# Kernel tuning notes

Hardware: AMD Instinct MI355X
Metric: run time of the kernel (lower is better)

Reference implementation:

```python
import jax, jax.numpy as jnp
import numpy as np

EPS = 1e-5
STW = 10   # short_term_window_size
L = 12     # mlp_layers


def gru_step(h, x, Wi, Wh, bi, bh):
    # torch nn.GRU cell, gate order (r, z, n)
    gi = x @ Wi.T + bi            # [B, 3H]
    gh = h @ Wh.T + bh            # [B, 3H]
    ir, iz, inn = jnp.split(gi, 3, axis=-1)
    hr, hz, hn = jnp.split(gh, 3, axis=-1)
    r = jax.nn.sigmoid(ir + hr)
    z = jax.nn.sigmoid(iz + hz)
    n = jnp.tanh(inn + r * hn)
    return (1.0 - z) * n + z * h


def mlp_mini(m, seq_W, seq_b, ln_a, ln_b, out_W, out_b, mrg_W, mrg_b):
    # m: [B, S, H] -> siMLPe_mini -> [B, 1, C]
    f = jnp.swapaxes(m, 1, 2)                 # [B, H, S]
    for l in range(L):                        # TransMLP: temporal FC + spatial LN + residual
        y = f @ seq_W[l].T + seq_b[l]         # Linear over seq axis S
        mu = y.mean(axis=1, keepdims=True)    # LN over feature ('spatial') axis H
        var = ((y - mu) ** 2).mean(axis=1, keepdims=True)
        y = (y - mu) / jnp.sqrt(var + EPS) * ln_a[l][None, :, None] + ln_b[l][None, :, None]
        f = f + y
    f = jnp.swapaxes(f, 1, 2) @ out_W.T + out_b   # [B, S, C]  motion_fc_out
    f = jnp.swapaxes(f, 1, 2) @ mrg_W.T + mrg_b   # [B, C, 1]  temporal_merge_fc
    return jnp.swapaxes(f, 1, 2)                  # [B, 1, C]


def _forward(x, gru_Wi, gru_Wh, gru_bi, gru_bh, enc_W, enc_b,
             seq_W, seq_b, ln_alpha, ln_beta, out_W, out_b, merge_W, merge_b):
    B, T, C = x.shape
    H = gru_Wh.shape[1]

    @jax.checkpoint
    def enc_step(h, xt):
        return gru_step(h, xt, gru_Wi, gru_Wh, gru_bi, gru_bh), None

    h0 = jnp.zeros((B, H), dtype=x.dtype)
    h_enc, _ = jax.lax.scan(enc_step, h0, jnp.swapaxes(x[:, :-1, :], 0, 1))

    last_frame = x[:, -1, :]
    # encode_history=True: one GRU step on the last frame; resulting state discarded
    window_history = gru_step(h_enc, last_frame, gru_Wi, gru_Wh, gru_bi, gru_bh)[:, None, :]  # [B,1,H]

    buf0 = x[:, -STW:, :]  # sliding short-term window buffer [B, STW, C]

    @jax.checkpoint
    def dec_step(carry, _):
        h, last, buf = carry
        h = gru_step(h, last, gru_Wi, gru_Wh, gru_bi, gru_bh)
        dec = h[:, None, :]                        # [B, 1, H]
        wst = buf @ enc_W.T + enc_b                # fc_encoder: [B, STW, H]
        mlp_in = jnp.concatenate([window_history, wst, dec], axis=1)  # [B, STW+2, H]
        new = mlp_mini(mlp_in, seq_W, seq_b, ln_alpha, ln_beta, out_W, out_b, mrg_W=merge_W, mrg_b=merge_b)
        new = new + last[:, None, :]               # recursive_residual=True
        newf = new[:, 0, :]
        buf = jnp.concatenate([buf[:, 1:, :], new], axis=1)
        return (h, newf, buf), newf

    _, outs = jax.lax.scan(dec_step, (h_enc, last_frame, buf0), None, length=T)
    return jnp.swapaxes(outs, 0, 1)  # [B, T, C]


def setup_inputs() -> dict:
    key = jax.random.key(0)
    B, T, C, H = 1024, 64, 66, 1024
    S = STW + 2
    ks = jax.random.split(key, 16)

    def g(k, shape, scale):
        return jax.random.normal(k, shape, dtype=jnp.float32) * scale

    return {
        "x": g(ks[0], (B, T, C), 1.0),
        "gru_Wi": g(ks[1], (3 * H, C), 0.05),
        "gru_Wh": g(ks[2], (3 * H, H), 0.02),
        "gru_bi": jnp.zeros((3 * H,), jnp.float32),
        "gru_bh": jnp.zeros((3 * H,), jnp.float32),
        "enc_W": g(ks[3], (H, C), 0.05),
        "enc_b": jnp.zeros((H,), jnp.float32),
        "seq_W": g(ks[4], (L, S, S), 0.2),
        "seq_b": jnp.zeros((L, S), jnp.float32),
        "ln_alpha": jnp.ones((L, H), jnp.float32),
        "ln_beta": jnp.zeros((L, H), jnp.float32),
        "out_W": g(ks[5], (C, H), 0.02),
        "out_b": jnp.zeros((C,), jnp.float32),
        "merge_W": g(ks[6], (1, S), 0.2),
        "merge_b": jnp.zeros((1,), jnp.float32),
    }


def reference(x, gru_Wi, gru_Wh, gru_bi, gru_bh, enc_W, enc_b,
              seq_W, seq_b, ln_alpha, ln_beta, out_W, out_b, merge_W, merge_b):
    return _forward(x, gru_Wi, gru_Wh, gru_bi, gru_bh, enc_W, enc_b,
                    seq_W, seq_b, ln_alpha, ln_beta, out_W, out_b, merge_W, merge_b)
```

## Files before the change

### kernel.cpp

```cpp
#include <hip/hip_runtime.h>
#include <hip/hip_bf16.h>
#include <cstddef>
#include <cstdint>

#define BB 1024
#define TT 64
#define CC 66
#define HH 1024
#define SS 12
#define LL 12
#define XROW (TT*CC)
#define DPSEG 32

typedef __attribute__((ext_vector_type(8))) __bf16 bfrag;
typedef __attribute__((ext_vector_type(4))) float f32x4;
typedef __attribute__((ext_vector_type(8))) short s8v;
typedef __attribute__((ext_vector_type(2))) float f2;

#define SWROW(r) (((r) >> 1) & 3)

__device__ __forceinline__ unsigned short f2bf(float f) {
  unsigned int u = __builtin_bit_cast(unsigned int, f);
  unsigned int r = u + 0x7FFFu + ((u >> 16) & 1u);
  return (unsigned short)(r >> 16);
}
__device__ __forceinline__ float bf2f(unsigned short h) {
  unsigned int u = ((unsigned int)h) << 16;
  return __builtin_bit_cast(float, u);
}

__device__ __forceinline__ void gload16(const void* g, void* l) {
  __builtin_amdgcn_global_load_lds(
      (const __attribute__((address_space(1))) unsigned int*)g,
      (__attribute__((address_space(3))) unsigned int*)l, 16, 0, 0);
}

template<int CTRL, int RM>
__device__ __forceinline__ float dppadd(float v) {
  int x = __builtin_amdgcn_update_dpp(0, __builtin_bit_cast(int, v),
                                      CTRL, RM, 0xF, true);
  return v + __builtin_bit_cast(float, x);
}
__device__ __forceinline__ float wave_sum63(float v) {
  v = dppadd<0x111, 0xF>(v);
  v = dppadd<0x112, 0xF>(v);
  v = dppadd<0x114, 0xF>(v);
  v = dppadd<0x118, 0xF>(v);
  v = dppadd<0x142, 0xa>(v);
  v = dppadd<0x143, 0xc>(v);
  return v;
}

__global__ __launch_bounds__(256) void gru_mfma(
    const unsigned short* __restrict__ Ahi, const unsigned short* __restrict__ Alo,
    const float* __restrict__ hprev,
    const unsigned short* __restrict__ Xhi, const unsigned short* __restrict__ Xlo,
    const unsigned short* __restrict__ Whi, const unsigned short* __restrict__ Wlo,
    const float* __restrict__ bi, const float* __restrict__ bh,
    float* __restrict__ hout_f32,
    unsigned short* __restrict__ hout_hi, unsigned short* __restrict__ hout_lo,
    const float* __restrict__ B144, float* __restrict__ dp32,
    const int* __restrict__ flagp, int do_dp)
{
  __shared__ __align__(16) unsigned short AsH[3][64*32];
  __shared__ __align__(16) unsigned short AsL[3][64*32];
  __shared__ __align__(16) unsigned short BsH[3][128*32];
  __shared__ __align__(16) unsigned short BsL[3][128*32];

  const int tid = threadIdx.x, lane = tid & 63, wid = tid >> 6;
  const int bid = blockIdx.x;
  const int idx = bid >> 3;
  const int jb = (bid & 7) * 4 + (idx & 3);
  const int b0 = (idx >> 2) * 64;
  const int wm = wid >> 1, wn = wid & 1;
  const int aR = lane >> 2, aC = lane & 3;

  auto stage = [&](int bs, int kc) {
    const unsigned short *shi, *slo; size_t go;
    int row = wid * 16 + aR;
    if (kc < 32) {
      go = (size_t)(b0 + row) * 1024 + (size_t)kc * 32 + aC * 8;
      shi = Ahi; slo = Alo;
    } else {
      go = (size_t)(b0 + row) * 96 + (size_t)(kc - 32) * 32 + aC * 8;
      shi = Xhi; slo = Xlo;
    }
    gload16(shi + go, &AsH[bs][wid * 512]);
    gload16(slo + go, &AsL[bs][wid * 512]);
    size_t base = ((size_t)jb * 35 + kc) * 4096;
    size_t go0 = base + (size_t)(wid * 32 + aR) * 32 + aC * 8;
    gload16(Whi + go0,       &BsH[bs][wid * 1024]);
    gload16(Whi + go0 + 512, &BsH[bs][wid * 1024 + 512]);
    gload16(Wlo + go0,       &BsL[bs][wid * 1024]);
    gload16(Wlo + go0 + 512, &BsL[bs][wid * 1024 + 512]);
  };

  int offA[2], offB[4];
  #pragma unroll
  for (int mh = 0; mh < 2; ++mh) {
    int r = wm * 32 + mh * 16 + (lane & 15);
    int cb = (lane >> 4) ^ SWROW(r);
    offA[mh] = r * 32 + cb * 8;
  }
  #pragma unroll
  for (int g = 0; g < 4; ++g) {
    int r = wn * 64 + g * 16 + (lane & 15);
    int cb = (lane >> 4) ^ SWROW(r);
    offB[g] = r * 32 + cb * 8;
  }

  f32x4 acc[2][4] = {};

  stage(0, 0);
  stage(1, 1);

  int cur = 0;
  for (int kc = 0; kc < 34; ++kc) {
    asm volatile("s_waitcnt vmcnt(6)" ::: "memory");
    __builtin_amdgcn_s_barrier();
    asm volatile("" ::: "memory");

    bfrag ah[2], al[2], bhf[4], blf[4];
    #pragma unroll
    for (int mh = 0; mh < 2; ++mh) {
      ah[mh] = __builtin_bit_cast(bfrag, *(const s8v*)(&AsH[cur][offA[mh]]));
      al[mh] = __builtin_bit_cast(bfrag, *(const s8v*)(&AsL[cur][offA[mh]]));
    }
    #pragma unroll
    for (int g = 0; g < 4; ++g) {
      bhf[g] = __builtin_bit_cast(bfrag, *(const s8v*)(&BsH[cur][offB[g]]));
      blf[g] = __builtin_bit_cast(bfrag, *(const s8v*)(&BsL[cur][offB[g]]));
    }
    if (kc < 33) {
      int st = (cur >= 1) ? cur - 1 : 2;
      stage(st, kc + 2);
    }
    #pragma unroll
    for (int mh = 0; mh < 2; ++mh)
      #pragma unroll
      for (int g = 0; g < 4; ++g) {
        acc[mh][g] = __builtin_amdgcn_mfma_f32_16x16x32_bf16(ah[mh], bhf[g], acc[mh][g], 0, 0, 0);
        acc[mh][g] = __builtin_amdgcn_mfma_f32_16x16x32_bf16(ah[mh], blf[g], acc[mh][g], 0, 0, 0);
        acc[mh][g] = __builtin_amdgcn_mfma_f32_16x16x32_bf16(al[mh], bhf[g], acc[mh][g], 0, 0, 0);
      }
    cur = (cur < 2) ? cur + 1 : 0;
  }
  {
    asm volatile("s_waitcnt vmcnt(0)" ::: "memory");
    __builtin_amdgcn_s_barrier();
    asm volatile("" ::: "memory");
    bfrag ah[2], al[2], bhf[4], blf[4];
    #pragma unroll
    for (int mh = 0; mh < 2; ++mh) {
      ah[mh] = __builtin_bit_cast(bfrag, *(const s8v*)(&AsH[1][offA[mh]]));
      al[mh] = __builtin_bit_cast(bfrag, *(const s8v*)(&AsL[1][offA[mh]]));
    }
    #pragma unroll
    for (int g = 0; g < 4; ++g) {
      bhf[g] = __builtin_bit_cast(bfrag, *(const s8v*)(&BsH[1][offB[g]]));
      blf[g] = __builtin_bit_cast(bfrag, *(const s8v*)(&BsL[1][offB[g]]));
    }
    #pragma unroll
    for (int mh = 0; mh < 2; ++mh)
      #pragma unroll
      for (int g = 0; g < 4; ++g) {
        acc[mh][g] = __builtin_amdgcn_mfma_f32_16x16x32_bf16(ah[mh], bhf[g], acc[mh][g], 0, 0, 0);
        acc[mh][g] = __builtin_amdgcn_mfma_f32_16x16x32_bf16(ah[mh], blf[g], acc[mh][g], 0, 0, 0);
        acc[mh][g] = __builtin_amdgcn_mfma_f32_16x16x32_bf16(al[mh], bhf[g], acc[mh][g], 0, 0, 0);
      }
  }

  const int j = jb * 32 + wn * 16 + (lane & 15);
  const float b_r  = bi[j] + bh[j];
  const float b_z  = bi[HH + j] + bh[HH + j];
  const float b_nh = bh[2 * HH + j];
  const float b_nx = bi[2 * HH + j];
  float hvv[2][4];
  #pragma unroll
  for (int mh = 0; mh < 2; ++mh)
    #pragma unroll
    for (int q = 0; q < 4; ++q) {
      int m = b0 + wm * 32 + mh * 16 + (lane >> 4) * 4 + q;
      float hpv = hprev[(size_t)m * HH + j];
      float rr = acc[mh][0][q] + b_r;
      float zz = acc[mh][1][q] + b_z;
      float nh = acc[mh][2][q] + b_nh;
      float nx = acc[mh][3][q] + b_nx;
      float r = 1.f / (1.f + __expf(-rr));
      float z = 1.f / (1.f + __expf(-zz));
      float n = tanhf(nx + r * nh);
      float hv = (1.f - z) * n + z * hpv;
      hvv[mh][q] = hv;
      hout_f32[(size_t)m * HH + j] = hv;
      unsigned short hi = f2bf(hv);
      float lo = hv - bf2f(hi);
      int cb = ((j >> 3) & 3) ^ SWROW(m);
      size_t dst = (size_t)m * 1024 + (size_t)(j & ~31) + cb * 8 + (j & 7);
      hout_hi[dst] = hi;
      hout_lo[dst] = f2bf(lo);
    }

  if (do_dp && *flagp) {
    float* hsf = reinterpret_cast<float*>(&AsH[0][0]);
    __syncthreads();
    #pragma unroll
    for (int mh = 0; mh < 2; ++mh)
      #pragma unroll
      for (int q = 0; q < 4; ++q) {
        int mloc = wm * 32 + mh * 16 + (lane >> 4) * 4 + q;
        int jloc = wn * 16 + (lane & 15);
        hsf[mloc * 33 + jloc] = hvv[mh][q];
      }
    __syncthreads();
    const int b_sub = tid & 63;
    const int cg = __builtin_amdgcn_readfirstlane(tid >> 6);
    const int base_c = cg * 36;
    float acc36[36];
    #pragma unroll
    for (int i = 0; i < 36; ++i) acc36[i] = 0.f;
    for (int kk = 0; kk < 32; ++kk) {
      float av = hsf[b_sub * 33 + kk];
      const float* brow = B144 + (size_t)(jb * 32 + kk) * 144 + base_c;
      #pragma unroll
      for (int qq = 0; qq < 9; ++qq) {
        f32x4 b4 = *(const f32x4*)(brow + qq * 4);
        acc36[qq*4+0] = fmaf(av, b4[0], acc36[qq*4+0]);
        acc36[qq*4+1] = fmaf(av, b4[1], acc36[qq*4+1]);
        acc36[qq*4+2] = fmaf(av, b4[2], acc36[qq*4+2]);
        acc36[qq*4+3] = fmaf(av, b4[3], acc36[qq*4+3]);
      }
    }
    float* drow = dp32 + ((size_t)jb * 1024 + b0 + b_sub) * 144 + base_c;
    #pragma unroll
    for (int qq = 0; qq < 9; ++qq)
      *(f32x4*)(drow + qq * 4) = { acc36[qq*4+0], acc36[qq*4+1], acc36[qq*4+2], acc36[qq*4+3] };
  }
}

__global__ __launch_bounds__(256) void prep_wgc(
    const float* __restrict__ Wh, const float* __restrict__ Wi,
    unsigned short* __restrict__ Whi, unsigned short* __restrict__ Wlo)
{
  size_t idx = (size_t)blockIdx.x * 256 + threadIdx.x;
  if (idx >= (size_t)4096 * 1120) return;
  int k = (int)(idx % 1120);
  int rg = (int)(idx / 1120);
  int jbv = rg >> 7, r = rg & 127;
  int jhi = r >> 6, rem = r & 63, g = rem >> 4, jlo = rem & 15;
  int j = jbv * 32 + jhi * 16 + jlo;
  float v = 0.f;
  if (g == 0)      v = (k < 1024) ? Wh[(size_t)j * HH + k]            : ((k < 1090) ? Wi[(size_t)j * CC + (k - 1024)] : 0.f);
  else if (g == 1) v = (k < 1024) ? Wh[(size_t)(HH + j) * HH + k]     : ((k < 1090) ? Wi[(size_t)(HH + j) * CC + (k - 1024)] : 0.f);
  else if (g == 2) v = (k < 1024) ? Wh[(size_t)(2 * HH + j) * HH + k] : 0.f;
  else             v = (k >= 1024 && k < 1090) ? Wi[(size_t)(2 * HH + j) * CC + (k - 1024)] : 0.f;
  unsigned short hi = f2bf(v);
  float lo = v - bf2f(hi);
  int kc = k >> 5, kk = k & 31;
  int cb = ((kk >> 3) ^ SWROW(r)) & 3;
  size_t dst = (((size_t)jbv * 35 + kc) * 128 + r) * 32 + cb * 8 + (kk & 7);
  Whi[dst] = hi;
  Wlo[dst] = f2bf(lo);
}

__global__ __launch_bounds__(256) void prep_xall(
    const float* __restrict__ x,
    unsigned short* __restrict__ Xhi, unsigned short* __restrict__ Xlo)
{
  size_t idx = (size_t)blockIdx.x * 256 + threadIdx.x;
  if (idx >= (size_t)TT * BB * 96) return;
  int kx = (int)(idx % 96);
  size_t rem = idx / 96;
  int b = (int)(rem % BB);
  int t = (int)(rem / BB);
  float v = (kx < CC) ? x[(size_t)b * XROW + (size_t)t * CC + kx] : 0.f;
  unsigned short hi = f2bf(v);
  float lo = v - bf2f(hi);
  int cb = (((kx >> 3) & 3) ^ SWROW(b)) & 3;
  size_t dst = ((size_t)t * BB + b) * 96 + (size_t)(kx & ~31) + cb * 8 + (kx & 7);
  Xhi[dst] = hi;
  Xlo[dst] = f2bf(lo);
}

__global__ __launch_bounds__(256) void wst_row_kernel(
    const float* __restrict__ src, int src_stride,
    const float* __restrict__ encWT, const float* __restrict__ encb,
    float* __restrict__ dst, const int* __restrict__ flagp)
{
  if (*flagp) return;
  __shared__ float s[CC];
  int b = blockIdx.y;
  int h = blockIdx.x * 256 + threadIdx.x;
  if (threadIdx.x < CC) s[threadIdx.x] = src[(size_t)b * src_stride + threadIdx.x];
  __syncthreads();
  float acc = encb[h];
  #pragma unroll
  for (int k = 0; k < CC; ++k) acc = fmaf(s[k], encWT[(size_t)k * HH + h], acc);
  dst[(size_t)b * (10 * HH) + h] = acc;
}

__global__ __launch_bounds__(256) void transpose_encW(
    const float* __restrict__ W, float* __restrict__ WT)
{
  int k = blockIdx.x;
  int h = blockIdx.y * 256 + threadIdx.x;
  WT[(size_t)k * HH + h] = W[(size_t)h * CC + k];
}

__global__ __launch_bounds__(256) void copy_last_kernel(
    const float* __restrict__ x, float* __restrict__ last)
{
  int idx = blockIdx.x * 256 + threadIdx.x;
  if (idx < BB * CC) {
    int b = idx / CC, c = idx - b * CC;
    last[idx] = x[(size_t)b * XROW + 63 * CC + c];
  }
}

__global__ __launch_bounds__(256) void flag_kernel(
    const float* __restrict__ lnA, const float* __restrict__ lnB, int* flagp)
{
  int idx = blockIdx.x * 256 + threadIdx.x;
  bool ok;
  if (idx < LL * HH) ok = (lnA[idx] == 1.0f);
  else ok = (lnB[idx - LL * HH] == 0.0f);
  if (!ok) atomicAnd(flagp, 0);
}

__global__ __launch_bounds__(256) void prep_tabs(
    const float* __restrict__ encW, const float* __restrict__ encb,
    const float* __restrict__ outW, float* __restrict__ tabs)
{
  const int lane = threadIdx.x & 63, wid = threadIdx.x >> 6;
  int idx = blockIdx.x * 4 + wid;
  if (idx >= 8978) return;
  float a = 0.f;
  if (idx < 4356) {
    int c1 = idx / 66, c2 = idx % 66;
    for (int h = lane; h < HH; h += 64) a = fmaf(encW[h * CC + c1], encW[h * CC + c2], a);
  } else if (idx < 8712) {
    int p = idx - 4356; int c = p / 66, c1 = p % 66;
    for (int h = lane; h < HH; h += 64) a = fmaf(encW[h * CC + c1], outW[(size_t)c * HH + h], a);
  } else if (idx < 8778) {
    int c1 = idx - 8712;
    for (int h = lane; h < HH; h += 64) a = fmaf(encW[h * CC + c1], encb[h], a);
  } else if (idx < 8844) {
    int c1 = idx - 8778;
    for (int h = lane; h < HH; h += 64) a += encW[h * CC + c1];
  } else if (idx < 8910) {
    int c = idx - 8844;
    for (int h = lane; h < HH; h += 64) a = fmaf(encb[h], outW[(size_t)c * HH + h], a);
  } else if (idx < 8976) {
    int c = idx - 8910;
    for (int h = lane; h < HH; h += 64) a += outW[(size_t)c * HH + h];
  } else if (idx == 8976) {
    for (int h = lane; h < HH; h += 64) a = fmaf(encb[h], encb[h], a);
  } else {
    for (int h = lane; h < HH; h += 64) a += encb[h];
  }
  a = wave_sum63(a);
  if (lane == 63) tabs[idx] = a;
}

__global__ __launch_bounds__(256) void prep_b144(
    const float* __restrict__ encW, const float* __restrict__ outW,
    const float* __restrict__ encb, float* __restrict__ B144)
{
  int idx = blockIdx.x * 256 + threadIdx.x;
  if (idx >= 1024 * 144) return;
  int k = idx / 144, n = idx % 144;
  float v;
  if (n < 66) v = encW[k * CC + n];
  else if (n < 132) v = outW[(size_t)(n - 66) * HH + k];
  else if (n == 132) v = encb[k];
  else if (n == 133) v = 1.f;
  else v = 0.f;
  B144[idx] = v;
}

__global__ __launch_bounds__(256) void linit_kernel(
    const float* __restrict__ x, float* __restrict__ l_ring,
    const int* __restrict__ flagp)
{
  if (!*flagp) return;
  int idx = blockIdx.x * 256 + threadIdx.x;
  if (idx >= 1024 * 9 * 66) return;
  int c = idx % 66; int r = idx / 66; int w = r % 9; int b = r / 9;
  l_ring[((size_t)b * 10 + w) * 66 + c] = x[(size_t)b * XROW + (54 + w) * CC + c];
}

__global__ __launch_bounds__(256) void qnew_kernel(
    const float* __restrict__ src, int sstride, const float* __restrict__ K3,
    float* __restrict__ q_ring, int slot, const int* __restrict__ flagp)
{
  if (!*flagp) return;
  __shared__ float Ks[4356];
  __shared__ float ls[8][66];
  int tid = threadIdx.x, b0 = blockIdx.x * 8;
  for (int i = tid; i < 4356; i += 256) Ks[i] = K3[i];
  for (int i = tid; i < 8 * 66; i += 256)
    ls[i / 66][i % 66] = src[(size_t)(b0 + i / 66) * sstride + (i % 66)];
  __syncthreads();
  for (int o = tid; o < 528; o += 256) {
    int bi = o / 66, c1 = o % 66;
    float a = 0.f;
    for (int c2 = 0; c2 < 66; ++c2) a = fmaf(Ks[c1 * 66 + c2], ls[bi][c2], a);
    q_ring[((size_t)(b0 + bi) * 10 + slot) * 66 + c1] = a;
  }
}

__global__ __launch_bounds__(256) void fast_combine(
    const float* __restrict__ dp, float* __restrict__ u, float* __restrict__ G,
    float* __restrict__ e, float* __restrict__ s, const int* __restrict__ flagp)
{
  if (!*flagp) return;
  int o = blockIdx.x * 256 + threadIdx.x;
  if (o >= 1024 * 144) return;
  int b = o / 144, c = o % 144;
  float a = 0.f;
  #pragma unroll
  for (int g = 0; g < DPSEG; ++g) a += dp[((size_t)g * 1024 + b) * 144 + c];
  if (c < 66) u[b * 66 + c] = a;
  else if (c < 132) G[b * 66 + (c - 66)] = a;
  else if (c == 132) e[b] = a;
  else if (c == 133) s[b] = a;
}

__global__ __launch_bounds__(256) void tail_kernel(
    const float* __restrict__ hdec, const float* __restrict__ whp,
    float* __restrict__ last, float* __restrict__ l_ring,
    float* __restrict__ q_ring, const float* __restrict__ dp,
    const float* __restrict__ u_whp, const float* __restrict__ G_whp,
    const float* __restrict__ e_whp, const float* __restrict__ s_whp,
    const float* __restrict__ tabs,
    float* __restrict__ wst, const float* __restrict__ encWT,
    const float* __restrict__ encb,
    const float* __restrict__ seqW, const float* __restrict__ seqb,
    const float* __restrict__ lnA, const float* __restrict__ lnB,
    const float* __restrict__ outW, const float* __restrict__ outb,
    const float* __restrict__ mrgW, const float* __restrict__ mrgb,
    int ring0, float* __restrict__ outp,
    unsigned short* __restrict__ lpH, unsigned short* __restrict__ lpL,
    const int* __restrict__ flagp)
{
  const int b = blockIdx.x, tid = threadIdx.x;
  const int lane = tid & 63, wid = tid >> 6;
  const int slot9 = (ring0 == 0) ? 9 : ring0 - 1;

  if (*flagp) {
    __shared__ float l_all[10][66], Qv[10][66];
    __shared__ float yd[66], gd[66], uw[66], se1[66], scs[66], lmix[66], newf[66];
    __shared__ float sW[156], sMm[156], sTt[156], sPp[156], sNn[156], sQq[156];
    __shared__ float sb12[12], sistd[12], scc[12], sfb[12], sdd12[12], swd[12], sVv[12], smrg[12];
    __shared__ float sred[12], misc[8];

    const float* K2T   = tabs + 4356;
    const float* tb_e1 = tabs + 8712;
    const float* tb_cs = tabs + 8778;
    const float* tb_g0 = tabs + 8844;
    const float* tb_R  = tabs + 8910;

    for (int i = tid; i < 660; i += 256) {
      int w = i / 66, c = i % 66;
      int slot = ring0 + w; if (slot >= 10) slot -= 10;
      Qv[w][c] = q_ring[((size_t)b * 10 + slot) * 66 + c];
      if (w < 9) l_all[w][c] = l_ring[((size_t)b * 10 + slot) * 66 + c];
      else       l_all[9][c] = last[(size_t)b * 66 + c];
    }
    for (int i = tid; i < 66; i += 256) {
      uw[i]  = u_whp[(size_t)b * 66 + i];
      se1[i] = tb_e1[i];
      scs[i] = tb_cs[i];
    }
    if (tid < 134) {
      float a = 0.f;
      #pragma unroll
      for (int g = 0; g < DPSEG; ++g) a += dp[((size_t)g * 1024 + b) * 144 + tid];
      if (tid < 66) yd[tid] = a;
      else if (tid < 132) gd[tid - 66] = a;
      else if (tid == 132) misc[1] = a;
      else misc[2] = a;
    }
    if (tid >= 160 && tid < 172) smrg[tid - 160] = mrgW[tid - 160];
    {
      f32x4 hv = *(const f32x4*)&hdec[(size_t)b * 1024 + tid * 4];
      f32x4 wv = *(const f32x4*)&whp[(size_t)b * 1024 + tid * 4];
      float d2 = hv[0]*hv[0] + hv[1]*hv[1] + hv[2]*hv[2] + hv[3]*hv[3];
      float dw = hv[0]*wv[0] + hv[1]*wv[1] + hv[2]*wv[2] + hv[3]*wv[3];
      float w2 = wv[0]*wv[0] + wv[1]*wv[1] + wv[2]*wv[2] + wv[3]*wv[3];
      d2 = wave_sum63(d2); dw = wave_sum63(dw); w2 = wave_sum63(w2);
      if (lane == 63) { sred[wid*3] = d2; sred[wid*3+1] = dw; sred[wid*3+2] = w2; }
    }
    __syncthreads();
    if (tid >= 128 && tid < 131) {
      int i = tid - 128;
      misc[3 + i] = sred[i] + sred[3 + i] + sred[6 + i] + sred[9 + i];
    }
    if (tid == 132) misc[6] = tabs[8976];
    if (tid == 133) misc[7] = tabs[8977];
    __syncthreads();

    if (tid < 144) {
      int i = tid / 12, j = tid % 12;
      float gv;
      if (i == 0 && j == 0) gv = misc[5];
      else if (i == 11 && j == 11) gv = misc[3];
      else if ((i == 0 && j == 11) || (i == 11 && j == 0)) gv = misc[4];
      else if (i == 0 || j == 0) {
        int w = (i == 0 ? j : i) - 1;
        float a = e_whp[b];
        for (int c = 0; c < 66; ++c) a = fmaf(uw[c], l_all[w][c], a);
        gv = a;
      } else if (i == 11 || j == 11) {
        int w = (i == 11 ? j : i) - 1;
        float a = misc[1];
        for (int c = 0; c < 66; ++c) a = fmaf(yd[c], l_all[w][c], a);
        gv = a;
      } else {
        int wi = i - 1, wj = j - 1;
        float a = misc[6];
        for (int c = 0; c < 66; ++c) a = fmaf(se1[c], l_all[wi][c] + l_all[wj][c], a);
        for (int c = 0; c < 66; ++c) a = fmaf(l_all[wi][c], Qv[wj][c], a);
        gv = a;
      }
      sMm[i * 13 + j] = gv * (1.f / 1024.f);
      sTt[i * 13 + j] = (i == j) ? 1.f : 0.f;
    }
    if (tid >= 144 && tid < 156) {
      int k = tid - 144;
      float fb;
      if (k == 0) fb = s_whp[b] * (1.f / 1024.f);
      else if (k == 11) fb = misc[2] * (1.f / 1024.f);
      else {
        float a = misc[7];
        for (int c = 0; c < 66; ++c) a = fmaf(scs[c], l_all[k - 1][c], a);
        fb = a * (1.f / 1024.f);
      }
      sfb[k] = fb;
      sdd12[k] = 0.f;
    }
    __syncthreads();

    for (int l = 0; l < LL; ++l) {
      if (tid < 144) sW[(tid / 12) * 13 + (tid % 12)] = seqW[l * 144 + tid];
      if (tid >= 160 && tid < 172) sb12[tid - 160] = seqb[l * 12 + (tid - 160)];
      __syncthreads();
      if (tid < 144) {
        int s = tid / 12, k = tid % 12;
        float a = 0.f;
        #pragma unroll
        for (int k2 = 0; k2 < 12; ++k2) a = fmaf(sW[s * 13 + k2], sMm[k2 * 13 + k], a);
        sPp[s * 13 + k] = a;
      }
      __syncthreads();
      if (tid < 12) {
        int s = tid;
        float mu = sb12[s];
        #pragma unroll
        for (int k = 0; k < 12; ++k) mu = fmaf(sW[s * 13 + k], sfb[k], mu);
        float e2 = 0.f;
        #pragma unroll
        for (int k = 0; k < 12; ++k) e2 = fmaf(sPp[s * 13 + k], sW[s * 13 + k], e2);
        float wf = mu - sb12[s];
        float var = fmaxf(e2 - wf * wf, 0.f);
        float is = 1.f / sqrtf(var + 1e-5f);
        sistd[s] = is;
        scc[s] = is * (sb12[s] - mu);
      }
      __syncthreads();
      if (tid < 144) {
        int i = tid / 12, j = tid % 12;
        float a = 0.f;
        #pragma unroll
        for (int k = 0; k < 12; ++k) a = fmaf(sW[i * 13 + k], sTt[k * 13 + j], a);
        sQq[i * 13 + j] = a;
        sNn[i * 13 + j] = sMm[i * 13 + j] + sistd[i] * sPp[i * 13 + j];
      }
      if (tid >= 144 && tid < 156) {
        int i = tid - 144;
        float a = 0.f;
        #pragma unroll
        for (int k = 0; k < 12; ++k) a = fmaf(sW[i * 13 + k], sdd12[k], a);
        swd[i] = a;
      }
      __syncthreads();
      if (tid < 144) {
        int i = tid / 12, j = tid % 12;
        sTt[i * 13 + j] += sistd[i] * sQq[i * 13 + j];
        float a = 0.f;
        #pragma unroll
        for (int k = 0; k < 12; ++k) a = fmaf(sNn[i * 13 + k], sW[j * 13 + k], a);
        sPp[i * 13 + j] = a;
      }
      if (tid >= 144 && tid < 156) {
        int i = tid - 144;
        sdd12[i] = sdd12[i] + sistd[i] * swd[i] + scc[i];
      }
      __syncthreads();
      if (tid < 144) {
        int i = tid / 12, j = tid % 12;
        sMm[i * 13 + j] = sNn[i * 13 + j] + sPp[i * 13 + j] * sistd[j]
                        + sfb[i] * scc[j] + scc[i] * sfb[j] - scc[i] * scc[j];
      }
      __syncthreads();
    }

    if (tid < 12) {
      float a = 0.f;
      #pragma unroll
      for (int s = 0; s < 12; ++s) a = fmaf(smrg[s], sTt[s * 13 + tid], a);
      sVv[tid] = a;
    }
    if (tid == 200) {
      float a = 0.f;
      for (int s = 0; s < 12; ++s) a = fmaf(smrg[s], sdd12[s], a);
      misc[0] = a;
    }
    __syncthreads();
    if (tid < 66) {
      float a = 0.f;
      #pragma unroll
      for (int w = 0; w < 9; ++w) a = fmaf(sVv[1 + w], l_all[w][tid], a);
      a = fmaf(sVv[10], l_all[9][tid], a);
      lmix[tid] = a;
    }
    __syncthreads();
    if (tid < 66) {
      int c = tid;
      float vsr = 0.f, smw = 0.f;
      #pragma unroll
      for (int k = 1; k <= 10; ++k) vsr += sVv[k];
      #pragma unroll
      for (int s = 0; s < 12; ++s) smw += smrg[s];
      float lastv = l_all[9][c];
      float acc = sVv[0] * G_whp[(size_t)b * 66 + c]
                + vsr * tb_g0[c]
                + sVv[11] * gd[c]
                + misc[0] * tb_R[c]
                + smw * outb[c] + mrgb[0] + lastv;
      const float* krow = K2T + c * 66;
      for (int c2 = 0; c2 < 66; ++c2) acc = fmaf(lmix[c2], krow[c2], acc);
      outp[(size_t)b * XROW + c] = acc;
      last[(size_t)b * 66 + c] = acc;
      l_ring[((size_t)b * 10 + slot9) * 66 + c] = lastv;
      newf[c] = acc;
      unsigned short hi = f2bf(acc);
      float lo = acc - bf2f(hi);
      int cb = (((c >> 3) & 3) ^ SWROW(b)) & 3;
      size_t dst = (size_t)b * 96 + (size_t)(c & ~31) + cb * 8 + (c & 7);
      lpH[dst] = hi;
      lpL[dst] = f2bf(lo);
    }
    __syncthreads();
    if (tid < 66) {
      float a = 0.f;
      const float* k3r = tabs + tid * 66;
      for (int c2 = 0; c2 < 66; ++c2) a = fmaf(k3r[c2], newf[c2], a);
      q_ring[((size_t)b * 10 + ring0) * 66 + tid] = a;
    }
    return;
  }

  __shared__ float red[4][24];
  __shared__ f2 mustd2[SS];
  __shared__ float g_lds[HH];
  __shared__ float nc[CC];

  const int h0 = tid;
  const int h1 = tid + 512;
  const float* lrow = last + (size_t)b * CC;
  f2 wnew[2];
  {
    f2 a0 = { encb[h0], encb[h0 + 256] };
    f2 a1 = { encb[h1], encb[h1 + 256] };
    #pragma unroll 11
    for (int k = 0; k < CC; ++k) {
      float lv = lrow[k];
      f2 lv2 = { lv, lv };
      f2 w0 = { encWT[(size_t)k * HH + h0], encWT[(size_t)k * HH + h0 + 256] };
      f2 w1 = { encWT[(size_t)k * HH + h1], encWT[(size_t)k * HH + h1 + 256] };
      a0 = __builtin_elementwise_fma(lv2, w0, a0);
      a1 = __builtin_elementwise_fma(lv2, w1, a1);
    }
    wnew[0] = a0; wnew[1] = a1;
    float* wd = wst + ((size_t)b * 10 + slot9) * HH;
    wd[h0] = a0.x; wd[h0 + 256] = a0.y;
    wd[h1] = a1.x; wd[h1 + 256] = a1.y;
  }

  f2 fr[2][SS];
  {
    const float* whb = whp + (size_t)b * HH;
    const float* hb  = hdec + (size_t)b * HH;
    fr[0][0]  = { whb[h0], whb[h0 + 256] };
    fr[1][0]  = { whb[h1], whb[h1 + 256] };
    fr[0][11] = { hb[h0], hb[h0 + 256] };
    fr[1][11] = { hb[h1], hb[h1 + 256] };
    #pragma unroll
    for (int w = 0; w < 9; ++w) {
      int slot = ring0 + w; if (slot >= 10) slot -= 10;
      const float* ws_ = wst + ((size_t)b * 10 + slot) * HH;
      fr[0][1 + w] = { ws_[h0], ws_[h0 + 256] };
      fr[1][1 + w] = { ws_[h1], ws_[h1 + 256] };
    }
    fr[0][10] = wnew[0];
    fr[1][10] = wnew[1];
  }

  #pragma unroll 1
  for (int l = 0; l < LL; ++l) {
    const float* W  = seqW + (size_t)l * SS * SS;
    const float* Bv = seqb + (size_t)l * SS;
    const float* lA = lnA + (size_t)l * HH;
    const float* lB = lnB + (size_t)l * HH;
    f2 al[2], be[2];
    al[0] = { lA[h0], lA[h0 + 256] };  al[1] = { lA[h1], lA[h1 + 256] };
    be[0] = { lB[h0], lB[h0 + 256] };  be[1] = { lB[h1], lB[h1 + 256] };

    f2 y[2][SS];
    #pragma unroll
    for (int s = 0; s < SS; ++s) {
      float bv = Bv[s];
      f2 a0 = { bv, bv }, a1 = { bv, bv };
      #pragma unroll
      for (int k = 0; k < SS; ++k) {
        float wv = W[s * SS + k];
        f2 wv2 = { wv, wv };
        a0 = __builtin_elementwise_fma(fr[0][k], wv2, a0);
        a1 = __builtin_elementwise_fma(fr[1][k], wv2, a1);
      }
      y[0][s] = a0; y[1][s] = a1;
      f2 pp = a0 + a1;
      float ps = wave_sum63(pp.x + pp.y);
      f2 qq = __builtin_elementwise_fma(a0, a0, a1 * a1);
      float pq = wave_sum63(qq.x + qq.y);
      if (lane == 63) { red[wid][s] = ps; red[wid][12 + s] = pq; }
    }
    __syncthreads();
    if (tid < SS) {
      float S = red[0][tid] + red[1][tid] + red[2][tid] + red[3][tid];
      float Q = red[0][12 + tid] + red[1][12 + tid] + red[2][12 + tid] + red[3][12 + tid];
      float mu = S * (1.f / HH);
      float var = Q * (1.f / HH) - mu * mu;
      mustd2[tid] = { mu, 1.f / sqrtf(var + 1e-5f) };
    }
    __syncthreads();
    #pragma unroll
    for (int s = 0; s < SS; ++s) {
      f2 mi = mustd2[s];
      f2 mus = { mi.x, mi.x };
      f2 isd = { mi.y, mi.y };
      #pragma unroll
      for (int p = 0; p < 2; ++p) {
        f2 t = (y[p][s] - mus) * isd;
        fr[p][s] = __builtin_elementwise_fma(t, al[p], fr[p][s]) + be[p];
      }
    }
    __syncthreads();
  }

  float smw = 0.f;
  f2 g[2] = { {0.f, 0.f}, {0.f, 0.f} };
  #pragma unroll
  for (int s = 0; s < SS; ++s) {
    float mv = mrgW[s];
    smw += mv;
    f2 mv2 = { mv, mv };
    g[0] = __builtin_elementwise_fma(mv2, fr[0][s], g[0]);
    g[1] = __builtin_elementwise_fma(mv2, fr[1][s], g[1]);
  }
  g_lds[h0] = g[0].x; g_lds[h0 + 256] = g[0].y;
  g_lds[h1] = g[1].x; g_lds[h1 + 256] = g[1].y;
  const float mbv = mrgb[0];
  __syncthreads();
  #pragma unroll 1
  for (int i = 0; i < 17; ++i) {
    int c = wid + 4 * i;
    if (c < CC) {
      const float* ow = outW + (size_t)c * HH;
      float acc = 0.f;
      #pragma unroll
      for (int q = 0; q < 16; ++q) acc = fmaf(g_lds[lane + q * 64], ow[lane + q * 64], acc);
      acc = wave_sum63(acc);
      if (lane == 63) nc[c] = acc + outb[c] * smw + mbv + lrow[c];
    }
  }
  __syncthreads();
  if (tid < CC) {
    float nv = nc[tid];
    outp[(size_t)b * XROW + tid] = nv;
    last[(size_t)b * CC + tid] = nv;
    unsigned short hi = f2bf(nv);
    float lo = nv - bf2f(hi);
    int cb = (((tid >> 3) & 3) ^ SWROW(b)) & 3;
    size_t dst = (size_t)b * 96 + (size_t)(tid & ~31) + cb * 8 + (tid & 7);
    lpH[dst] = hi;
    lpL[dst] = f2bf(lo);
  }
}

extern "C" void kernel_launch(void* const* d_in, const int* in_sizes, int n_in,
                              void* d_out, int out_size, void* d_ws, size_t ws_size,
                              hipStream_t stream) {
  const float* x    = (const float*)d_in[0];
  const float* gWi  = (const float*)d_in[1];
  const float* gWh  = (const float*)d_in[2];
  const float* gbi  = (const float*)d_in[3];
  const float* gbh  = (const float*)d_in[4];
  const float* encW = (const float*)d_in[5];
  const float* encb = (const float*)d_in[6];
  const float* seqW = (const float*)d_in[7];
  const float* seqb = (const float*)d_in[8];
  const float* lnA  = (const float*)d_in[9];
  const float* lnB  = (const float*)d_in[10];
  const float* outW = (const float*)d_in[11];
  const float* outb = (const float*)d_in[12];
  const float* mrgW = (const float*)d_in[13];
  const float* mrgb = (const float*)d_in[14];
  float* out = (float*)d_out;

  char* p = (char*)d_ws;
  auto alloc = [&](size_t bytes) { char* r = p; p += (bytes + 255) & ~(size_t)255; return r; };
  float* encWT = (float*)alloc((size_t)CC * HH * 4);
  float* last  = (float*)alloc((size_t)BB * CC * 4);
  float* wst   = (float*)alloc((size_t)BB * 10 * HH * 4);
  float* hf[3];
  for (int i = 0; i < 3; ++i) hf[i] = (float*)alloc((size_t)BB * HH * 4);
  unsigned short* WgH = (unsigned short*)alloc((size_t)4096 * 1120 * 2);
  unsigned short* WgL = (unsigned short*)alloc((size_t)4096 * 1120 * 2);
  unsigned short* XaH = (unsigned short*)alloc((size_t)TT * BB * 96 * 2);
  unsigned short* XaL = (unsigned short*)alloc((size_t)TT * BB * 96 * 2);
  unsigned short* hhi[3]; unsigned short* hlo[3];
  for (int i = 0; i < 3; ++i) {
    hhi[i] = (unsigned short*)alloc((size_t)BB * HH * 2);
    hlo[i] = (unsigned short*)alloc((size_t)BB * HH * 2);
  }
  unsigned short* lpH = (unsigned short*)alloc((size_t)BB * 96 * 2);
  unsigned short* lpL = (unsigned short*)alloc((size_t)BB * 96 * 2);
  int* flag = (int*)alloc(256);
  if ((size_t)(p - (char*)d_ws) > ws_size) return;

  char* ov = (char*)wst;
  float* B144  = (float*)ov;                 ov += (size_t)1024 * 144 * 4;
  float* dp32  = (float*)ov;                 ov += (size_t)DPSEG * 1024 * 144 * 4;
  float* l_ring= (float*)ov;                 ov += (size_t)1024 * 10 * 66 * 4;
  float* q_ring= (float*)ov;                 ov += (size_t)1024 * 10 * 66 * 4;
  float* u_whp = (float*)ov;                 ov += (size_t)1024 * 66 * 4;
  float* G_whp = (float*)ov;                 ov += (size_t)1024 * 66 * 4;
  float* e_whp = (float*)ov;                 ov += 4096;
  float* s_whp = (float*)ov;                 ov += 4096;
  float* tabs  = (float*)ov;                 ov += 9216 * 4;

  hipMemsetAsync(flag, 0xFF, 4, stream);
  flag_kernel<<<dim3(96), 256, 0, stream>>>(lnA, lnB, flag);
  prep_wgc<<<dim3((4096u * 1120u) / 256u), 256, 0, stream>>>(gWh, gWi, WgH, WgL);
  prep_xall<<<dim3(((unsigned)TT * BB * 96) / 256u), 256, 0, stream>>>(x, XaH, XaL);
  transpose_encW<<<dim3(CC, HH/256), 256, 0, stream>>>(encW, encWT);
  copy_last_kernel<<<dim3((BB*CC + 255)/256), 256, 0, stream>>>(x, last);
  prep_b144<<<dim3(576), 256, 0, stream>>>(encW, outW, encb, B144);
  prep_tabs<<<dim3(2245), 256, 0, stream>>>(encW, encb, outW, tabs);
  linit_kernel<<<dim3((1024*9*66)/256), 256, 0, stream>>>(x, l_ring, flag);
  for (int w = 0; w < 10; ++w)
    qnew_kernel<<<dim3(128), 256, 0, stream>>>(x + (size_t)(54 + w) * CC, XROW,
                                               tabs, q_ring, w, flag);
  hipMemsetAsync(hf[0], 0, (size_t)BB * HH * 4, stream);
  hipMemsetAsync(hhi[0], 0, (size_t)BB * HH * 2, stream);
  hipMemsetAsync(hlo[0], 0, (size_t)BB * HH * 2, stream);

  const dim3 ggrid(512);

  int cur = 0;
  for (int t = 0; t < 63; ++t) {
    int nxt = 1 - cur;
    gru_mfma<<<ggrid, 256, 0, stream>>>(
        hhi[cur], hlo[cur], hf[cur],
        XaH + (size_t)t * BB * 96, XaL + (size_t)t * BB * 96,
        WgH, WgL, gbi, gbh, hf[nxt], hhi[nxt], hlo[nxt],
        B144, dp32, flag, 0);
    cur = nxt;
  }
  gru_mfma<<<ggrid, 256, 0, stream>>>(
      hhi[cur], hlo[cur], hf[cur],
      XaH + (size_t)63 * BB * 96, XaL + (size_t)63 * BB * 96,
      WgH, WgL, gbi, gbh, hf[2], hhi[2], hlo[2],
      B144, dp32, flag, 1);

  fast_combine<<<dim3(576), 256, 0, stream>>>(dp32, u_whp, G_whp, e_whp, s_whp, flag);

  for (int w = 0; w < 9; ++w)
    wst_row_kernel<<<dim3(HH/256, BB), 256, 0, stream>>>(
        x + (size_t)(54 + w) * CC, XROW, encWT, encb, wst + (size_t)w * HH, flag);

  int hc = 2;
  for (int t = 0; t < 64; ++t) {
    if (t > 0) {
      int hn = (t - 1) & 1;
      gru_mfma<<<ggrid, 256, 0, stream>>>(
          hhi[hc], hlo[hc], hf[hc], lpH, lpL,
          WgH, WgL, gbi, gbh, hf[hn], hhi[hn], hlo[hn],
          B144, dp32, flag, 1);
      hc = hn;
    }
    tail_kernel<<<dim3(BB), 256, 0, stream>>>(
        hf[hc], hf[2], last, l_ring, q_ring, dp32,
        u_whp, G_whp, e_whp, s_whp, tabs,
        wst, encWT, encb, seqW, seqb, lnA, lnB, outW, outb, mrgW, mrgb,
        t % 10, out + (size_t)t * CC, lpH, lpL, flag);
  }
}
```

Baseline: 7.953 ms.

## Run tail 12x12 recurrence in a single wavefront and transpose dp partial layout

The fast-path tail kernel now preloads all layers' seq weights into LDS and runs the 12-layer 12x12 moment recurrence on wave 0 only, replacing the many block-wide barriers with an LDS wait. Two of the per-layer phases are merged and M is double-buffered. The dp partial-sum buffer is re-laid out so each batch row's 32 segments are contiguous, which makes the reductions read one contiguous block. The single-wave path relies on implicit intra-wave ordering of LDS accesses and leaves 3 of 4 waves idle.

After: 7.623 ms (median of 2 runs). 1.04x faster.

```diff
diff --git a/kernel.cpp b/kernel.cpp
--- a/kernel.cpp
+++ b/kernel.cpp
@@ -18,6 +18,7 @@
 typedef __attribute__((ext_vector_type(2))) float f2;
 
 #define SWROW(r) (((r) >> 1) & 3)
+#define WSYNC() asm volatile("s_waitcnt lgkmcnt(0)" ::: "memory")
 
 __device__ __forceinline__ unsigned short f2bf(float f) {
   unsigned int u = __builtin_bit_cast(unsigned int, f);
@@ -230,7 +231,7 @@
         acc36[qq*4+3] = fmaf(av, b4[3], acc36[qq*4+3]);
       }
     }
-    float* drow = dp32 + ((size_t)jb * 1024 + b0 + b_sub) * 144 + base_c;
+    float* drow = dp32 + ((size_t)(b0 + b_sub) * 32 + jb) * 144 + base_c;
     #pragma unroll
     for (int qq = 0; qq < 9; ++qq)
       *(f32x4*)(drow + qq * 4) = { acc36[qq*4+0], acc36[qq*4+1], acc36[qq*4+2], acc36[qq*4+3] };
@@ -418,7 +419,7 @@
   int b = o / 144, c = o % 144;
   float a = 0.f;
   #pragma unroll
-  for (int g = 0; g < DPSEG; ++g) a += dp[((size_t)g * 1024 + b) * 144 + c];
+  for (int g = 0; g < DPSEG; ++g) a += dp[((size_t)b * 32 + g) * 144 + c];
   if (c < 66) u[b * 66 + c] = a;
   else if (c < 132) G[b * 66 + (c - 66)] = a;
   else if (c == 132) e[b] = a;
@@ -449,8 +450,9 @@
   if (*flagp) {
     __shared__ float l_all[10][66], Qv[10][66];
     __shared__ float yd[66], gd[66], uw[66], se1[66], scs[66], lmix[66], newf[66];
-    __shared__ float sW[156], sMm[156], sTt[156], sPp[156], sNn[156], sQq[156];
-    __shared__ float sb12[12], sistd[12], scc[12], sfb[12], sdd12[12], swd[12], sVv[12], smrg[12];
+    __shared__ float sWall[LL * 156];
+    __shared__ float sMa[156], sMb[156], sTt[156], sPp[156], sQq[156];
+    __shared__ float sfb[16], sdd[16], swd[16], sistd[16], sccv[16], sVv[16], smrg[16];
     __shared__ float sred[12], misc[8];
 
     const float* K2T   = tabs + 4356;
@@ -471,15 +473,21 @@
       se1[i] = tb_e1[i];
       scs[i] = tb_cs[i];
     }
+    for (int i = tid; i < LL * 144; i += 256) {
+      int l = i / 144, e = i % 144;
+      sWall[l * 156 + (e / 12) * 13 + (e % 12)] = seqW[i];
+    }
     if (tid < 134) {
       float a = 0.f;
       #pragma unroll
-      for (int g = 0; g < DPSEG; ++g) a += dp[((size_t)g * 1024 + b) * 144 + tid];
+      for (int g = 0; g < DPSEG; ++g) a += dp[((size_t)b * 32 + g) * 144 + tid];
       if (tid < 66) yd[tid] = a;
       else if (tid < 132) gd[tid - 66] = a;
       else if (tid == 132) misc[1] = a;
       else misc[2] = a;
     }
+    if (tid == 134) misc[6] = tabs[8976];
+    if (tid == 135) misc[7] = tabs[8977];
     if (tid >= 160 && tid < 172) smrg[tid - 160] = mrgW[tid - 160];
     {
       f32x4 hv = *(const f32x4*)&hdec[(size_t)b * 1024 + tid * 4];
@@ -491,141 +499,143 @@
       if (lane == 63) { sred[wid*3] = d2; sred[wid*3+1] = dw; sred[wid*3+2] = w2; }
     }
     __syncthreads();
-    if (tid >= 128 && tid < 131) {
-      int i = tid - 128;
-      misc[3 + i] = sred[i] + sred[3 + i] + sred[6 + i] + sred[9 + i];
-    }
-    if (tid == 132) misc[6] = tabs[8976];
-    if (tid == 133) misc[7] = tabs[8977];
-    __syncthreads();
-
-    if (tid < 144) {
-      int i = tid / 12, j = tid % 12;
-      float gv;
-      if (i == 0 && j == 0) gv = misc[5];
-      else if (i == 11 && j == 11) gv = misc[3];
-      else if ((i == 0 && j == 11) || (i == 11 && j == 0)) gv = misc[4];
-      else if (i == 0 || j == 0) {
-        int w = (i == 0 ? j : i) - 1;
-        float a = e_whp[b];
-        for (int c = 0; c < 66; ++c) a = fmaf(uw[c], l_all[w][c], a);
-        gv = a;
-      } else if (i == 11 || j == 11) {
-        int w = (i == 11 ? j : i) - 1;
-        float a = misc[1];
-        for (int c = 0; c < 66; ++c) a = fmaf(yd[c], l_all[w][c], a);
-        gv = a;
-      } else {
-        int wi = i - 1, wj = j - 1;
-        float a = misc[6];
-        for (int c = 0; c < 66; ++c) a = fmaf(se1[c], l_all[wi][c] + l_all[wj][c], a);
-        for (int c = 0; c < 66; ++c) a = fmaf(l_all[wi][c], Qv[wj][c], a);
-        gv = a;
+    if (wid != 0) return;
+
+    if (lane < 3) misc[3 + lane] = sred[lane] + sred[3 + lane] + sred[6 + lane] + sred[9 + lane];
+    WSYNC();
+
+    #pragma unroll
+    for (int rep = 0; rep < 3; ++rep) {
+      int e = lane + rep * 64;
+      if (e < 144) {
+        int i = e / 12, j = e % 12;
+        float gv;
+        if (i == 0 && j == 0) gv = misc[5];
+        else if (i == 11 && j == 11) gv = misc[3];
+        else if ((i == 0 && j == 11) || (i == 11 && j == 0)) gv = misc[4];
+        else if (i == 0 || j == 0) {
+          int w = (i == 0 ? j : i) - 1;
+          float a = e_whp[b];
+          for (int c = 0; c < 66; ++c) a = fmaf(uw[c], l_all[w][c], a);
+          gv = a;
+        } else if (i == 11 || j == 11) {
+          int w = (i == 11 ? j : i) - 1;
+          float a = misc[1];
+          for (int c = 0; c < 66; ++c) a = fmaf(yd[c], l_all[w][c], a);
+          gv = a;
+        } else {
+          int wi = i - 1, wj = j - 1;
+          float a = misc[6];
+          for (int c = 0; c < 66; ++c) a = fmaf(se1[c], l_all[wi][c] + l_all[wj][c], a);
+          for (int c = 0; c < 66; ++c) a = fmaf(l_all[wi][c], Qv[wj][c], a);
+          gv = a;
+        }
+        sMa[i * 13 + j] = gv * (1.f / 1024.f);
+        sTt[i * 13 + j] = (i == j) ? 1.f : 0.f;
+      } else if (e < 156) {
+        int k = e - 144;
+        float fb;
+        if (k == 0) fb = s_whp[b] * (1.f / 1024.f);
+        else if (k == 11) fb = misc[2] * (1.f / 1024.f);
+        else {
+          float a = misc[7];
+          for (int c = 0; c < 66; ++c) a = fmaf(scs[c], l_all[k - 1][c], a);
+          fb = a * (1.f / 1024.f);
+        }
+        sfb[k] = fb;
+        sdd[k] = 0.f;
       }
-      sMm[i * 13 + j] = gv * (1.f / 1024.f);
-      sTt[i * 13 + j] = (i == j) ? 1.f : 0.f;
-    }
-    if (tid >= 144 && tid < 156) {
-      int k = tid - 144;
-      float fb;
-      if (k == 0) fb = s_whp[b] * (1.f / 1024.f);
-      else if (k == 11) fb = misc[2] * (1.f / 1024.f);
-      else {
-        float a = misc[7];
-        for (int c = 0; c < 66; ++c) a = fmaf(scs[c], l_all[k - 1][c], a);
-        fb = a * (1.f / 1024.f);
+    }
+    WSYNC();
+
+    for (int l = 0; l < LL; ++l) {
+      const float* Wl = sWall + l * 156;
+      float* Mr = (l & 1) ? sMb : sMa;
+      float* Mw = (l & 1) ? sMa : sMb;
+      #pragma unroll
+      for (int rep = 0; rep < 3; ++rep) {
+        int e = lane + rep * 64;
+        if (e < 144) {
+          int i = e / 12, j = e % 12;
+          float ap = 0.f, aq = 0.f;
+          #pragma unroll
+          for (int k = 0; k < 12; ++k) {
+            float wv = Wl[i * 13 + k];
+            ap = fmaf(wv, Mr[k * 13 + j], ap);
+            aq = fmaf(wv, sTt[k * 13 + j], aq);
+          }
+          sPp[i * 13 + j] = ap;
+          sQq[i * 13 + j] = aq;
+        } else if (e < 156) {
+          int i = e - 144;
+          float a = 0.f;
+          #pragma unroll
+          for (int k = 0; k < 12; ++k) a = fmaf(Wl[i * 13 + k], sdd[k], a);
+          swd[i] = a;
+        }
       }
-      sfb[k] = fb;
-      sdd12[k] = 0.f;
-    }
-    __syncthreads();
-
-    for (int l = 0; l < LL; ++l) {
-      if (tid < 144) sW[(tid / 12) * 13 + (tid % 12)] = seqW[l * 144 + tid];
-      if (tid >= 160 && tid < 172) sb12[tid - 160] = seqb[l * 12 + (tid - 160)];
-      __syncthreads();
-      if (tid < 144) {
-        int s = tid / 12, k = tid % 12;
-        float a = 0.f;
+      WSYNC();
+      if (lane < 12) {
+        int s = lane;
+        float bv = seqb[l * 12 + s];
+        float mu = bv;
         #pragma unroll
-        for (int k2 = 0; k2 < 12; ++k2) a = fmaf(sW[s * 13 + k2], sMm[k2 * 13 + k], a);
-        sPp[s * 13 + k] = a;
-      }
-      __syncthreads();
-      if (tid < 12) {
-        int s = tid;
-        float mu = sb12[s];
-        #pragma unroll
-        for (int k = 0; k < 12; ++k) mu = fmaf(sW[s * 13 + k], sfb[k], mu);
+        for (int k = 0; k < 12; ++k) mu = fmaf(Wl[s * 13 + k], sfb[k], mu);
         float e2 = 0.f;
         #pragma unroll
-        for (int k = 0; k < 12; ++k) e2 = fmaf(sPp[s * 13 + k], sW[s * 13 + k], e2);
-        float wf = mu - sb12[s];
+        for (int k = 0; k < 12; ++k) e2 = fmaf(sPp[s * 13 + k], Wl[s * 13 + k], e2);
+        float wf = mu - bv;
         float var = fmaxf(e2 - wf * wf, 0.f);
         float is = 1.f / sqrtf(var + 1e-5f);
         sistd[s] = is;
-        scc[s] = is * (sb12[s] - mu);
+        sccv[s] = is * (bv - mu);
       }
-      __syncthreads();
-      if (tid < 144) {
-        int i = tid / 12, j = tid % 12;
-        float a = 0.f;
-        #pragma unroll
-        for (int k = 0; k < 12; ++k) a = fmaf(sW[i * 13 + k], sTt[k * 13 + j], a);
-        sQq[i * 13 + j] = a;
-        sNn[i * 13 + j] = sMm[i * 13 + j] + sistd[i] * sPp[i * 13 + j];
+      WSYNC();
+      #pragma unroll
+      for (int rep = 0; rep < 3; ++rep) {
+        int e = lane + rep * 64;
+        if (e < 144) {
+          int i = e / 12, j = e % 12;
+          float Di = sistd[i];
+          sTt[i * 13 + j] += Di * sQq[i * 13 + j];
+          float p2 = 0.f;
+          #pragma unroll
+          for (int k = 0; k < 12; ++k) {
+            float n_ik = Mr[i * 13 + k] + Di * sPp[i * 13 + k];
+            p2 = fmaf(n_ik, Wl[j * 13 + k], p2);
+          }
+          float n_ij = Mr[i * 13 + j] + Di * sPp[i * 13 + j];
+          Mw[i * 13 + j] = n_ij + p2 * sistd[j]
+                         + sfb[i] * sccv[j] + sccv[i] * sfb[j] - sccv[i] * sccv[j];
+        } else if (e < 156) {
+          int i = e - 144;
+          sdd[i] = sdd[i] + sistd[i] * swd[i] + sccv[i];
+        }
       }
-      if (tid >= 144 && tid < 156) {
-        int i = tid - 144;
-        float a = 0.f;
-        #pragma unroll
-        for (int k = 0; k < 12; ++k) a = fmaf(sW[i * 13 + k], sdd12[k], a);
-        swd[i] = a;
-      }
-      __syncthreads();
-      if (tid < 144) {
-        int i = tid / 12, j = tid % 12;
-        sTt[i * 13 + j] += sistd[i] * sQq[i * 13 + j];
-        float a = 0.f;
-        #pragma unroll
-        for (int k = 0; k < 12; ++k) a = fmaf(sNn[i * 13 + k], sW[j * 13 + k], a);
-        sPp[i * 13 + j] = a;
-      }
-      if (tid >= 144 && tid < 156) {
-        int i = tid - 144;
-        sdd12[i] = sdd12[i] + sistd[i] * swd[i] + scc[i];
-      }
-      __syncthreads();
-      if (tid < 144) {
-        int i = tid / 12, j = tid % 12;
-        sMm[i * 13 + j] = sNn[i * 13 + j] + sPp[i * 13 + j] * sistd[j]
-                        + sfb[i] * scc[j] + scc[i] * sfb[j] - scc[i] * scc[j];
-      }
-      __syncthreads();
-    }
-
-    if (tid < 12) {
+      WSYNC();
+    }
+
+    if (lane < 12) {
       float a = 0.f;
       #pragma unroll
-      for (int s = 0; s < 12; ++s) a = fmaf(smrg[s], sTt[s * 13 + tid], a);
-      sVv[tid] = a;
-    }
-    if (tid == 200) {
+      for (int s = 0; s < 12; ++s) a = fmaf(smrg[s], sTt[s * 13 + lane], a);
+      sVv[lane] = a;
+    }
+    if (lane == 12) {
       float a = 0.f;
-      for (int s = 0; s < 12; ++s) a = fmaf(smrg[s], sdd12[s], a);
+      for (int s = 0; s < 12; ++s) a = fmaf(smrg[s], sdd[s], a);
       misc[0] = a;
     }
-    __syncthreads();
-    if (tid < 66) {
+    WSYNC();
+    for (int c = lane; c < 66; c += 64) {
       float a = 0.f;
       #pragma unroll
-      for (int w = 0; w < 9; ++w) a = fmaf(sVv[1 + w], l_all[w][tid], a);
-      a = fmaf(sVv[10], l_all[9][tid], a);
-      lmix[tid] = a;
-    }
-    __syncthreads();
-    if (tid < 66) {
-      int c = tid;
+      for (int w = 0; w < 9; ++w) a = fmaf(sVv[1 + w], l_all[w][c], a);
+      a = fmaf(sVv[10], l_all[9][c], a);
+      lmix[c] = a;
+    }
+    WSYNC();
+    for (int c = lane; c < 66; c += 64) {
       float vsr = 0.f, smw = 0.f;
       #pragma unroll
       for (int k = 1; k <= 10; ++k) vsr += sVv[k];
@@ -650,12 +660,12 @@
       lpH[dst] = hi;
       lpL[dst] = f2bf(lo);
     }
-    __syncthreads();
-    if (tid < 66) {
+    WSYNC();
+    for (int c = lane; c < 66; c += 64) {
       float a = 0.f;
-      const float* k3r = tabs + tid * 66;
+      const float* k3r = tabs + c * 66;
       for (int c2 = 0; c2 < 66; ++c2) a = fmaf(k3r[c2], newf[c2], a);
-      q_ring[((size_t)b * 10 + ring0) * 66 + tid] = a;
+      q_ring[((size_t)b * 10 + ring0) * 66 + c] = a;
     }
     return;
   }
```
